# Kernel tuning notes

Measured on AMD Instinct MI355X. Metric: run time of the kernel, lower is better.

The kernel has to match this reference:

```python
import jax, jax.numpy as jnp
import numpy as np

B, T, D = 2, 2048, 2048
H, KVH = 16, 4
HD = D // H            # 128
HALF = HD // 2         # 64
EPS = 1e-6


def zc_rmsnorm(x, scale):
    # zero-centred RMSNorm: (1+scale) * x / rms(x), rms in fp32
    rms = jnp.sqrt(jnp.mean(x.astype(jnp.float32) ** 2, axis=-1, keepdims=True) + EPS)
    return ((1.0 + scale) * x / rms).astype(x.dtype)


def apply_rope(x, cos, sin):
    # x: [B, h, T, HD]; cos/sin: [T, HALF]
    t = x.shape[2]
    c = cos[:t][None, None, :, :]
    s = sin[:t][None, None, :, :]
    x1, x2 = x[..., :HALF], x[..., HALF:]
    return jnp.concatenate([x1 * c - x2 * s, x2 * c + x1 * s], axis=-1)


def setup_inputs() -> dict:
    key = jax.random.key(0)
    ks = jax.random.split(key, 8)
    std = 0.02
    res_std = 0.02 / np.sqrt(2 * 24)
    q_input = jax.random.normal(ks[0], (B, T, D), jnp.float32)
    kv_input = jax.random.normal(ks[1], (B, T, D), jnp.float32)
    mask = jnp.tril(jnp.ones((T, T), bool))[None, None, :, :]
    inv_freq = 1.0 / (10000.0 ** (jnp.arange(0, HALF, dtype=jnp.float32) / HALF))
    ang = jnp.arange(T, dtype=jnp.float32)[:, None] * inv_freq[None, :]
    cos, sin = jnp.cos(ang), jnp.sin(ang)
    Wq = jax.random.normal(ks[2], (D, D), jnp.float32) * std
    Wk = jax.random.normal(ks[3], (D, KVH * HD), jnp.float32) * std
    Wv = jax.random.normal(ks[4], (D, KVH * HD), jnp.float32) * std
    q_scale = jnp.zeros((HD,), jnp.float32)
    k_scale = jnp.zeros((HD,), jnp.float32)
    Wo = jax.random.normal(ks[5], (D, D), jnp.float32) * res_std
    return {"q_input": q_input, "kv_input": kv_input, "mask": mask,
            "cos": cos, "sin": sin, "Wq": Wq, "Wk": Wk, "Wv": Wv,
            "q_scale": q_scale, "k_scale": k_scale, "Wo": Wo}


def reference(q_input, kv_input, mask, cos, sin, Wq, Wk, Wv, q_scale, k_scale, Wo):
    b = q_input.shape[0]
    q = (q_input @ Wq).reshape(b, -1, H, HD).transpose(0, 2, 1, 3)      # [B,H,T,HD]
    k = (kv_input @ Wk).reshape(b, -1, KVH, HD).transpose(0, 2, 1, 3)   # [B,KVH,T,HD]
    v = (kv_input @ Wv).reshape(b, -1, KVH, HD).transpose(0, 2, 1, 3)
    q = zc_rmsnorm(q, q_scale)
    k = zc_rmsnorm(k, k_scale)
    rep = H // KVH
    k = jnp.repeat(k, rep, axis=1)
    v = jnp.repeat(v, rep, axis=1)
    q = apply_rope(q, cos, sin)
    k = apply_rope(k, cos, sin)
    scale = jnp.sqrt(jnp.float32(HD))
    scores = jnp.einsum('bhqd,bhkd->bhqk', q, k) / scale                # [B,H,T,T]
    scores = jnp.where(mask, scores, jnp.finfo(scores.dtype).min)
    attn = jax.nn.softmax(scores, axis=-1)
    out = jnp.einsum('bhqk,bhkd->bhqd', attn, v)
    out = out.transpose(0, 2, 1, 3).reshape(b, -1, D)
    return out @ Wo
```

## Files before the change

### kernel.cpp

```cpp
#include <hip/hip_runtime.h>

#define NB 2
#define NT 2048
#define ND 2048
#define NH 16
#define NKVH 4
#define NHD 128
#define NHALF 64
#define NREP (NH / NKVH)
#define MFIX 12.0f

typedef __bf16 bf16x8 __attribute__((ext_vector_type(8)));
typedef unsigned short u16x8 __attribute__((ext_vector_type(8)));
typedef float f32x4 __attribute__((ext_vector_type(4)));

__device__ __forceinline__ unsigned short f2b(float f) {
  union { float f; unsigned int u; } v; v.f = f;
  unsigned int r = v.u + 0x7FFFu + ((v.u >> 16) & 1u);
  return (unsigned short)(r >> 16);
}
__device__ __forceinline__ float b2f(unsigned short h) {
  union { unsigned int u; float f; } v; v.u = ((unsigned int)h) << 16;
  return v.f;
}

__device__ __forceinline__ void glds16(const unsigned short* g, unsigned short* l) {
  __builtin_amdgcn_global_load_lds(
      (__attribute__((address_space(1))) unsigned int*)(unsigned long long)g,
      (__attribute__((address_space(3))) unsigned int*)(unsigned int)(unsigned long long)l,
      16, 0, 0);
}

__global__ __launch_bounds__(256) void f2bf(const float* __restrict__ in,
                                            unsigned short* __restrict__ out) {
  const size_t i = (size_t)(blockIdx.x * 256 + threadIdx.x) * 8;
  float4 a = *(const float4*)(in + i);
  float4 b = *(const float4*)(in + i + 4);
  u16x8 r;
  r[0] = f2b(a.x); r[1] = f2b(a.y); r[2] = f2b(a.z); r[3] = f2b(a.w);
  r[4] = f2b(b.x); r[5] = f2b(b.y); r[6] = f2b(b.z); r[7] = f2b(b.w);
  *(u16x8*)(out + i) = r;
}

__global__ __launch_bounds__(256) void wtrans(const float* __restrict__ in,
                                              unsigned short* __restrict__ out,
                                              int K, int N) {
  __shared__ float tile[32][33];
  const int k0 = blockIdx.y * 32, n0 = blockIdx.x * 32;
  const int x = threadIdx.x & 31, y8 = threadIdx.x >> 5;
#pragma unroll
  for (int j = 0; j < 4; ++j) {
    const int y = y8 + j * 8;
    tile[y][x] = in[(size_t)(k0 + y) * N + n0 + x];
  }
  __syncthreads();
#pragma unroll
  for (int j = 0; j < 4; ++j) {
    const int y = y8 + j * 8;
    out[(size_t)(n0 + y) * K + k0 + x] = f2b(tile[x][y]);
  }
}

__global__ __launch_bounds__(256) void gemm128(const unsigned short* __restrict__ A,
                                               const unsigned short* __restrict__ Bt,
                                               float* __restrict__ C,
                                               int M, int N, int K) {
  __shared__ unsigned short As[128 * 32];
  __shared__ unsigned short Bs[128 * 32];
  const int tid = threadIdx.x;
  const int wave = tid >> 6, lane = tid & 63;
  const int wm = wave >> 1, wn = wave & 1;
  const int quad = lane >> 4, c = lane & 15;
  const int m0 = blockIdx.y * 128, n0 = blockIdx.x * 128;
  const int gr = lane >> 2;
  const int gc = (lane & 3) * 8;

  const unsigned short* pa0 = A + (size_t)(m0 + wave * 16 + gr) * K + gc;
  const unsigned short* pa1 = A + (size_t)(m0 + 64 + wave * 16 + gr) * K + gc;
  const unsigned short* pb0 = Bt + (size_t)(n0 + wave * 16 + gr) * K + gc;
  const unsigned short* pb1 = Bt + (size_t)(n0 + 64 + wave * 16 + gr) * K + gc;
  unsigned short* la0 = &As[(wave * 16) * 32];
  unsigned short* la1 = &As[(64 + wave * 16) * 32];
  unsigned short* lb0 = &Bs[(wave * 16) * 32];
  unsigned short* lb1 = &Bs[(64 + wave * 16) * 32];

  f32x4 acc[4][4] = {};

  for (int k0 = 0; k0 < K; k0 += 32) {
    glds16(pa0 + k0, la0);
    glds16(pa1 + k0, la1);
    glds16(pb0 + k0, lb0);
    glds16(pb1 + k0, lb1);
    __syncthreads();
    bf16x8 af[4];
#pragma unroll
    for (int sm = 0; sm < 4; ++sm)
      af[sm] = *(const bf16x8*)&As[(wm * 64 + sm * 16 + c) * 32 + quad * 8];
#pragma unroll
    for (int sn = 0; sn < 4; ++sn) {
      bf16x8 bfr = *(const bf16x8*)&Bs[(wn * 64 + sn * 16 + c) * 32 + quad * 8];
#pragma unroll
      for (int sm = 0; sm < 4; ++sm)
        acc[sm][sn] = __builtin_amdgcn_mfma_f32_16x16x32_bf16(af[sm], bfr, acc[sm][sn], 0, 0, 0);
    }
    __syncthreads();
  }

#pragma unroll
  for (int sm = 0; sm < 4; ++sm)
#pragma unroll
    for (int sn = 0; sn < 4; ++sn) {
      const int row = m0 + wm * 64 + sm * 16 + quad * 4;
      const int col = n0 + wn * 64 + sn * 16 + c;
#pragma unroll
      for (int r = 0; r < 4; ++r)
        C[(size_t)(row + r) * N + col] = acc[sm][sn][r];
    }
}

__global__ __launch_bounds__(256) void rmsnorm_rope(const float* __restrict__ in,
                                                    unsigned short* __restrict__ out,
                                                    const float* __restrict__ scale,
                                                    const float* __restrict__ cosp,
                                                    const float* __restrict__ sinp,
                                                    int nh, int instride, float outscale) {
  const int wid = blockIdx.x * 4 + (threadIdx.x >> 6);
  const int lane = threadIdx.x & 63;
  const int h = wid % nh;
  const int t = (wid / nh) % NT;
  const int b = wid / (nh * NT);
  const float* x = in + (size_t)(b * NT + t) * instride + h * NHD;
  float x1 = x[lane], x2 = x[lane + NHALF];
  float ss = x1 * x1 + x2 * x2;
#pragma unroll
  for (int m = 1; m < 64; m <<= 1) ss += __shfl_xor(ss, m, 64);
  const float inv = 1.0f / sqrtf(ss * (1.0f / NHD) + 1e-6f);
  const float n1 = (1.0f + scale[lane]) * x1 * inv;
  const float n2 = (1.0f + scale[lane + NHALF]) * x2 * inv;
  const float cc = cosp[t * NHALF + lane], s = sinp[t * NHALF + lane];
  const size_t ob = (((size_t)b * nh + h) * NT + t) * NHD;
  out[ob + lane] = f2b((n1 * cc - n2 * s) * outscale);
  out[ob + lane + NHALF] = f2b((n2 * cc + n1 * s) * outscale);
}

__global__ __launch_bounds__(256) void vtrans(const float* __restrict__ in,
                                              unsigned short* __restrict__ out,
                                              int instride) {
  __shared__ float tile[32][33];
  const int bg = blockIdx.z;
  const int b = bg >> 2, g = bg & 3;
  const int t0 = blockIdx.x * 32, d0 = blockIdx.y * 32;
  const int x = threadIdx.x & 31, y8 = threadIdx.x >> 5;
#pragma unroll
  for (int j = 0; j < 4; ++j) {
    const int y = y8 + j * 8;
    tile[y][x] = in[(size_t)(b * NT + t0 + y) * instride + g * NHD + d0 + x];
  }
  __syncthreads();
#pragma unroll
  for (int j = 0; j < 4; ++j) {
    const int y = y8 + j * 8;
    out[((size_t)bg * NHD + d0 + y) * NT + t0 + x] = f2b(tile[x][y]);
  }
}

__global__ __launch_bounds__(256, 3) void attn64(const unsigned short* __restrict__ Qh,
                                                 const unsigned short* __restrict__ Kh,
                                                 const unsigned short* __restrict__ Vtg,
                                                 unsigned short* __restrict__ O) {
  __shared__ unsigned short Kt[64 * 132];
  __shared__ unsigned short Vt[128 * 68];
  __shared__ unsigned short Pt[64 * 68];
  const int bh = blockIdx.x;
  const int b = bh / NH, h = bh % NH, g = h / NREP;
  const int y = blockIdx.y;
  const int a = y & 7, bb = y >> 3;
  const int qt = (bb == 0) ? a : (bb == 1) ? a + 8 : (bb == 2) ? 31 - a : 23 - a;
  const int tid = threadIdx.x;
  const int w = tid >> 6, lane = tid & 63;
  const int quad = lane >> 4, c = lane & 15;

  bf16x8 qf[4];
  {
    const unsigned short* qp =
        Qh + ((size_t)(b * NH + h) * NT + qt * 64 + w * 16 + c) * NHD + quad * 8;
#pragma unroll
    for (int ch = 0; ch < 4; ++ch) qf[ch] = *(const bf16x8*)(qp + ch * 32);
  }

  f32x4 acc_o[8] = {};
  float lsum[4] = {0.f, 0.f, 0.f, 0.f};
  const size_t kbase = (size_t)(b * NKVH + g) * NT * NHD;
  const size_t vbase = (size_t)(b * NKVH + g) * NHD * NT;
  const int nkt = qt + 1;

  u16x8 kreg[4], vreg[4];
#pragma unroll
  for (int j = 0; j < 4; ++j) {
    const int f = j * 256 + tid;
    kreg[j] = *(const u16x8*)&Kh[kbase + (size_t)(f >> 4) * NHD + (f & 15) * 8];
    vreg[j] = *(const u16x8*)&Vtg[vbase + (size_t)(f >> 3) * NT + (f & 7) * 8];
  }

  for (int kt = 0; kt < nkt; ++kt) {
#pragma unroll
    for (int j = 0; j < 4; ++j) {
      const int f = j * 256 + tid;
      *(u16x8*)&Kt[(f >> 4) * 132 + (f & 15) * 8] = kreg[j];
      *(u16x8*)&Vt[(f >> 3) * 68 + (f & 7) * 8] = vreg[j];
    }
    __syncthreads();

    if (kt + 1 < nkt) {
      const int k0 = (kt + 1) * 64;
#pragma unroll
      for (int j = 0; j < 4; ++j) {
        const int f = j * 256 + tid;
        kreg[j] = *(const u16x8*)&Kh[kbase + (size_t)(k0 + (f >> 4)) * NHD + (f & 15) * 8];
        vreg[j] = *(const u16x8*)&Vtg[vbase + (size_t)(f >> 3) * NT + k0 + (f & 7) * 8];
      }
    }

    f32x4 s[4] = {};
#pragma unroll
    for (int n = 0; n < 4; ++n)
#pragma unroll
      for (int ch = 0; ch < 4; ++ch) {
        bf16x8 kf = *(const bf16x8*)&Kt[(n * 16 + c) * 132 + ch * 32 + quad * 8];
        s[n] = __builtin_amdgcn_mfma_f32_16x16x32_bf16(qf[ch], kf, s[n], 0, 0, 0);
      }

    const bool dmask = (kt == qt);
#pragma unroll
    for (int r = 0; r < 4; ++r) {
      float v0 = s[0][r], v1 = s[1][r], v2 = s[2][r], v3 = s[3][r];
      const int lrow = w * 16 + quad * 4 + r;
      if (dmask) {
        if (c > lrow) v0 = -1e30f;
        if (16 + c > lrow) v1 = -1e30f;
        if (32 + c > lrow) v2 = -1e30f;
        if (48 + c > lrow) v3 = -1e30f;
      }
      const float p0 = __expf(v0 - MFIX), p1 = __expf(v1 - MFIX);
      const float p2 = __expf(v2 - MFIX), p3 = __expf(v3 - MFIX);
      lsum[r] += (p0 + p1) + (p2 + p3);
      Pt[lrow * 68 + c] = f2b(p0);
      Pt[lrow * 68 + 16 + c] = f2b(p1);
      Pt[lrow * 68 + 32 + c] = f2b(p2);
      Pt[lrow * 68 + 48 + c] = f2b(p3);
    }

#pragma unroll
    for (int kc2 = 0; kc2 < 2; ++kc2) {
      bf16x8 pf = *(const bf16x8*)&Pt[(w * 16 + c) * 68 + kc2 * 32 + quad * 8];
#pragma unroll
      for (int n2 = 0; n2 < 8; ++n2) {
        bf16x8 vf = *(const bf16x8*)&Vt[(n2 * 16 + c) * 68 + kc2 * 32 + quad * 8];
        acc_o[n2] = __builtin_amdgcn_mfma_f32_16x16x32_bf16(pf, vf, acc_o[n2], 0, 0, 0);
      }
    }
    __syncthreads();
  }

#pragma unroll
  for (int r = 0; r < 4; ++r) {
    float l = lsum[r];
    l += __shfl_xor(l, 1, 64);
    l += __shfl_xor(l, 2, 64);
    l += __shfl_xor(l, 4, 64);
    l += __shfl_xor(l, 8, 64);
    lsum[r] = l;
  }

#pragma unroll
  for (int r = 0; r < 4; ++r) {
    const float invl = 1.0f / lsum[r];
    const int qrow = qt * 64 + w * 16 + quad * 4 + r;
    unsigned short* op = O + ((size_t)(b * NT + qrow) * NH + h) * NHD + c;
#pragma unroll
    for (int n2 = 0; n2 < 8; ++n2) op[n2 * 16] = f2b(acc_o[n2][r] * invl);
  }
}

extern "C" void kernel_launch(void* const* d_in, const int* in_sizes, int n_in,
                              void* d_out, int out_size, void* d_ws, size_t ws_size,
                              hipStream_t stream) {
  (void)in_sizes; (void)n_in; (void)out_size; (void)ws_size;
  const float* q_input  = (const float*)d_in[0];
  const float* kv_input = (const float*)d_in[1];
  const float* cosp = (const float*)d_in[3];
  const float* sinp = (const float*)d_in[4];
  const float* Wq = (const float*)d_in[5];
  const float* Wk = (const float*)d_in[6];
  const float* Wv = (const float*)d_in[7];
  const float* q_scale = (const float*)d_in[8];
  const float* k_scale = (const float*)d_in[9];
  const float* Wo = (const float*)d_in[10];
  float* out = (float*)d_out;

  char* p = (char*)d_ws;
  float* Q32  = (float*)p; p += (size_t)NB * NT * ND * 4;
  float* KVp  = (float*)p; p += (size_t)NB * NT * 1024 * 4;
  unsigned short* Qb16  = (unsigned short*)p; p += (size_t)NB * NT * ND * 2;
  unsigned short* KVb16 = (unsigned short*)p; p += (size_t)NB * NT * ND * 2;
  unsigned short* Kh  = (unsigned short*)p; p += (size_t)NB * NKVH * NT * NHD * 2;
  unsigned short* Vtg = (unsigned short*)p; p += (size_t)NB * NKVH * NT * NHD * 2;
  unsigned short* Wqt  = (unsigned short*)p; p += (size_t)ND * ND * 2;
  unsigned short* WkvT = (unsigned short*)p; p += (size_t)1024 * ND * 2;
  unsigned short* Wot  = (unsigned short*)p; p += (size_t)ND * ND * 2;
  unsigned short* Ob = Qb16;
  unsigned short* Qh = KVb16;

  const dim3 blk(256);
  const int M = NB * NT;

  f2bf<<<dim3(M * ND / 2048), blk, 0, stream>>>(q_input, Qb16);
  f2bf<<<dim3(M * ND / 2048), blk, 0, stream>>>(kv_input, KVb16);

  wtrans<<<dim3(ND / 32, ND / 32), blk, 0, stream>>>(Wq, Wqt, ND, ND);
  wtrans<<<dim3(512 / 32, ND / 32), blk, 0, stream>>>(Wk, WkvT, ND, 512);
  wtrans<<<dim3(512 / 32, ND / 32), blk, 0, stream>>>(Wv, WkvT + (size_t)512 * ND, ND, 512);
  wtrans<<<dim3(ND / 32, ND / 32), blk, 0, stream>>>(Wo, Wot, ND, ND);

  gemm128<<<dim3(ND / 128, M / 128), blk, 0, stream>>>(Qb16, Wqt, Q32, M, ND, ND);
  gemm128<<<dim3(1024 / 128, M / 128), blk, 0, stream>>>(KVb16, WkvT, KVp, M, 1024, ND);

  rmsnorm_rope<<<dim3(NB * NT * NH / 4), blk, 0, stream>>>(Q32, Qh, q_scale, cosp, sinp,
                                                           NH, ND, 0.08838834764831845f);
  rmsnorm_rope<<<dim3(NB * NT * NKVH / 4), blk, 0, stream>>>(KVp, Kh, k_scale, cosp, sinp,
                                                             NKVH, 1024, 1.0f);
  vtrans<<<dim3(NT / 32, NHD / 32, NB * NKVH), blk, 0, stream>>>(KVp + 512, Vtg, 1024);

  attn64<<<dim3(NB * NH, 32), blk, 0, stream>>>(Qh, Kh, Vtg, Ob);

  gemm128<<<dim3(ND / 128, M / 128), blk, 0, stream>>>(Ob, Wot, out, M, ND, ND);
}
```

Measured before the change: 426.3 us.

## Double-buffer GEMM LDS tiles and remap workgroups across XCDs

The bf16 GEMM kernel now keeps two LDS buffers and issues the global-to-LDS loads for the next K-step before running the MFMAs on the current one. This overlaps memory latency with compute and drops one barrier per iteration. The block index is also remapped so consecutive tiles interleave across the 8 XCDs, which may improve L2 locality. The cost is doubled LDS use, which can lower occupancy. The remap assumes the workgroup count is a multiple of 8.

```diff
diff --git a/kernel.cpp b/kernel.cpp
--- a/kernel.cpp
+++ b/kernel.cpp
@@ -65,45 +65,55 @@
                                                const unsigned short* __restrict__ Bt,
                                                float* __restrict__ C,
                                                int M, int N, int K) {
-  __shared__ unsigned short As[128 * 32];
-  __shared__ unsigned short Bs[128 * 32];
+  __shared__ unsigned short As[2][128 * 32];
+  __shared__ unsigned short Bs[2][128 * 32];
   const int tid = threadIdx.x;
   const int wave = tid >> 6, lane = tid & 63;
   const int wm = wave >> 1, wn = wave & 1;
   const int quad = lane >> 4, c = lane & 15;
-  const int m0 = blockIdx.y * 128, n0 = blockIdx.x * 128;
-  const int gr = lane >> 2;
-  const int gc = (lane & 3) * 8;
-
-  const unsigned short* pa0 = A + (size_t)(m0 + wave * 16 + gr) * K + gc;
-  const unsigned short* pa1 = A + (size_t)(m0 + 64 + wave * 16 + gr) * K + gc;
-  const unsigned short* pb0 = Bt + (size_t)(n0 + wave * 16 + gr) * K + gc;
-  const unsigned short* pb1 = Bt + (size_t)(n0 + 64 + wave * 16 + gr) * K + gc;
-  unsigned short* la0 = &As[(wave * 16) * 32];
-  unsigned short* la1 = &As[(64 + wave * 16) * 32];
-  unsigned short* lb0 = &Bs[(wave * 16) * 32];
-  unsigned short* lb1 = &Bs[(64 + wave * 16) * 32];
+
+  const int gx = gridDim.x;
+  const int nwg = gx * gridDim.y;
+  int lin = blockIdx.y * gx + blockIdx.x;
+  lin = (lin & 7) * (nwg >> 3) + (lin >> 3);
+  const int m0 = (lin / gx) * 128, n0 = (lin % gx) * 128;
+
+  const unsigned short* pa0 = A + (size_t)(m0 + wave * 16 + (lane >> 2)) * K + (lane & 3) * 8;
+  const unsigned short* pa1 = pa0 + (size_t)64 * K;
+  const unsigned short* pb0 = Bt + (size_t)(n0 + wave * 16 + (lane >> 2)) * K + (lane & 3) * 8;
+  const unsigned short* pb1 = pb0 + (size_t)64 * K;
 
   f32x4 acc[4][4] = {};
 
-  for (int k0 = 0; k0 < K; k0 += 32) {
-    glds16(pa0 + k0, la0);
-    glds16(pa1 + k0, la1);
-    glds16(pb0 + k0, lb0);
-    glds16(pb1 + k0, lb1);
-    __syncthreads();
+  const int nsteps = K >> 5;
+  int cur = 0;
+  glds16(pa0, &As[0][(wave * 16) * 32]);
+  glds16(pa1, &As[0][(64 + wave * 16) * 32]);
+  glds16(pb0, &Bs[0][(wave * 16) * 32]);
+  glds16(pb1, &Bs[0][(64 + wave * 16) * 32]);
+  __syncthreads();
+
+  for (int t = 0; t < nsteps; ++t) {
+    if (t + 1 < nsteps) {
+      const int kn = (t + 1) << 5;
+      glds16(pa0 + kn, &As[cur ^ 1][(wave * 16) * 32]);
+      glds16(pa1 + kn, &As[cur ^ 1][(64 + wave * 16) * 32]);
+      glds16(pb0 + kn, &Bs[cur ^ 1][(wave * 16) * 32]);
+      glds16(pb1 + kn, &Bs[cur ^ 1][(64 + wave * 16) * 32]);
+    }
     bf16x8 af[4];
 #pragma unroll
     for (int sm = 0; sm < 4; ++sm)
-      af[sm] = *(const bf16x8*)&As[(wm * 64 + sm * 16 + c) * 32 + quad * 8];
+      af[sm] = *(const bf16x8*)&As[cur][(wm * 64 + sm * 16 + c) * 32 + quad * 8];
 #pragma unroll
     for (int sn = 0; sn < 4; ++sn) {
-      bf16x8 bfr = *(const bf16x8*)&Bs[(wn * 64 + sn * 16 + c) * 32 + quad * 8];
+      bf16x8 bfr = *(const bf16x8*)&Bs[cur][(wn * 64 + sn * 16 + c) * 32 + quad * 8];
 #pragma unroll
       for (int sm = 0; sm < 4; ++sm)
         acc[sm][sn] = __builtin_amdgcn_mfma_f32_16x16x32_bf16(af[sm], bfr, acc[sm][sn], 0, 0, 0);
     }
     __syncthreads();
+    cur ^= 1;
   }
 
 #pragma unroll
```

After: 385.8 us. -9.5%, faster.
